# Optimization experiments

Measured on AMD Instinct MI355X. Metric: run time of the kernel, lower is better.

## Reference

```python
import jax, jax.numpy as jnp
import numpy as np

N, E, DIN, DOUT = 100000, 1600000, 64, 64
P_DROP = 0.1


def setup_inputs() -> dict:
    key = jax.random.key(0)
    k1, k2, k3 = jax.random.split(key, 3)
    x = jax.random.normal(k1, (N, DIN), dtype=jnp.float32)
    W = jax.random.normal(k2, (DIN, DOUT), dtype=jnp.float32) / np.sqrt(DIN)
    b = jnp.zeros((DOUT,), dtype=jnp.float32)
    edge_index = jax.random.randint(k3, (2, E), 0, N, dtype=jnp.int32)
    return {"x": x, "W": W, "b": b, "edge_index": edge_index}


def reference(x, W, b, edge_index):
    # PyG GCNConv semantics: add self-loops, symmetric normalization,
    # linear transform first, aggregate at target (edge_index[1]), bias after.
    row, col = edge_index[0], edge_index[1]
    loops = jnp.arange(N, dtype=edge_index.dtype)
    row = jnp.concatenate([row, loops])  # [E+N] source nodes
    col = jnp.concatenate([col, loops])  # [E+N] target nodes

    deg = jax.ops.segment_sum(jnp.ones_like(col, dtype=x.dtype), col, num_segments=N)
    dinv = jax.lax.rsqrt(jnp.maximum(deg, 1.0))  # self-loops guarantee deg >= 1
    norm = dinv[row] * dinv[col]  # [E+N]

    xw = x @ W  # [N, DOUT] small GEMM before scatter
    msg = xw[row] * norm[:, None]  # [E+N, DOUT] gather + scale
    agg = jax.ops.segment_sum(msg, col, num_segments=N) + b  # scatter-add

    h = jnp.tanh(agg)
    keep = jax.random.bernoulli(jax.random.key(42), 1.0 - P_DROP, h.shape)
    return jnp.where(keep, h / (1.0 - P_DROP), 0.0)
```

## Files before the change

### kernel.cpp

```cpp
#include <hip/hip_runtime.h>
#include <hip/hip_bf16.h>


#define NN 100000
#define NE 1600000
#define NBUCK 1563
#define P1B 256
#define P1T 1024
#define CHUNK 6250
#define CAP 1152
#define SPILLCAP 16384
#define HCAP 1536

typedef __attribute__((ext_vector_type(8))) short bf8;
typedef __attribute__((ext_vector_type(4))) float f32x4;

__device__ __forceinline__ unsigned rotl32(unsigned x, int r) {
    return (x << r) | (x >> (32 - r));
}

__device__ __forceinline__ void threefry2x32(unsigned k0, unsigned k1,
                                             unsigned x0, unsigned x1,
                                             unsigned& o0, unsigned& o1) {
    const unsigned ks0 = k0, ks1 = k1, ks2 = k0 ^ k1 ^ 0x1BD11BDAu;
    x0 += ks0; x1 += ks1;
    x0 += x1; x1 = rotl32(x1, 13); x1 ^= x0;
    x0 += x1; x1 = rotl32(x1, 15); x1 ^= x0;
    x0 += x1; x1 = rotl32(x1, 26); x1 ^= x0;
    x0 += x1; x1 = rotl32(x1, 6);  x1 ^= x0;
    x0 += ks1; x1 += ks2 + 1u;
    x0 += x1; x1 = rotl32(x1, 17); x1 ^= x0;
    x0 += x1; x1 = rotl32(x1, 29); x1 ^= x0;
    x0 += x1; x1 = rotl32(x1, 16); x1 ^= x0;
    x0 += x1; x1 = rotl32(x1, 24); x1 ^= x0;
    x0 += ks2; x1 += ks0 + 2u;
    x0 += x1; x1 = rotl32(x1, 13); x1 ^= x0;
    x0 += x1; x1 = rotl32(x1, 15); x1 ^= x0;
    x0 += x1; x1 = rotl32(x1, 26); x1 ^= x0;
    x0 += x1; x1 = rotl32(x1, 6);  x1 ^= x0;
    x0 += ks0; x1 += ks1 + 3u;
    x0 += x1; x1 = rotl32(x1, 17); x1 ^= x0;
    x0 += x1; x1 = rotl32(x1, 29); x1 ^= x0;
    x0 += x1; x1 = rotl32(x1, 16); x1 ^= x0;
    x0 += x1; x1 = rotl32(x1, 24); x1 ^= x0;
    x0 += ks1; x1 += ks2 + 4u;
    x0 += x1; x1 = rotl32(x1, 13); x1 ^= x0;
    x0 += x1; x1 = rotl32(x1, 15); x1 ^= x0;
    x0 += x1; x1 = rotl32(x1, 26); x1 ^= x0;
    x0 += x1; x1 = rotl32(x1, 6);  x1 ^= x0;
    x0 += ks2; x1 += ks0 + 5u;
    o0 = x0; o1 = x1;
}

__device__ __forceinline__ void sagg_finish(float4 a0, float4 a1, int lane,
                                            int c, float dv, float bv,
                                            float* __restrict__ out) {
    float ax = a0.x + a1.x, ay = a0.y + a1.y;
    float az = a0.z + a1.z, aw = a0.w + a1.w;
    ax += __shfl_xor(ax, 16); ax += __shfl_xor(ax, 32);
    ay += __shfl_xor(ay, 16); ay += __shfl_xor(ay, 32);
    az += __shfl_xor(az, 16); az += __shfl_xor(az, 32);
    aw += __shfl_xor(aw, 16); aw += __shfl_xor(aw, 32);
    const float sx = __shfl(ax, lane >> 2);
    const float sy = __shfl(ay, lane >> 2);
    const float sz = __shfl(az, lane >> 2);
    const float sw = __shfl(aw, lane >> 2);
    const float ab = (lane & 1) ? sy : sx;
    const float cd = (lane & 1) ? sw : sz;
    const float a = (lane & 2) ? cd : ab;
    const int p = c * 64 + lane;
    unsigned o0, o1;
    threefry2x32(0u, 42u, 0u, (unsigned)p, o0, o1);
    const unsigned bits = o0 ^ o1;
    const float u = __uint_as_float((bits >> 9) | 0x3f800000u) - 1.0f;
    const float h = tanhf(dv * a + bv);
    out[p] = (u < 0.9f) ? h / 0.9f : 0.0f;
}

#define UNPK4(v, A)                                                    \
    A.x += __uint_as_float((v).x << 16);                               \
    A.y += __uint_as_float((v).x & 0xffff0000u);                       \
    A.z += __uint_as_float((v).y << 16);                               \
    A.w += __uint_as_float((v).y & 0xffff0000u);

__global__ __launch_bounds__(P1T) void k_p1(const int* __restrict__ ei,
                                            int* __restrict__ gcur,
                                            unsigned* __restrict__ packed,
                                            unsigned* __restrict__ spill_pk,
                                            unsigned* __restrict__ spill_bk,
                                            int* __restrict__ gspill) {
    __shared__ int hb[NBUCK];
    __shared__ int lc[NBUCK];
    const int tid = threadIdx.x;
    for (int i = tid; i < NBUCK; i += P1T) { hb[i] = 0; lc[i] = 0; }
    __syncthreads();
    const int base = blockIdx.x * CHUNK;
    for (int i = tid; i < CHUNK; i += P1T) {
        const unsigned t = (unsigned)ei[NE + base + i];
        if (t < NN) atomicAdd(&hb[t >> 6], 1);
    }
    __syncthreads();
    for (int i = tid; i < NBUCK; i += P1T) {
        const int h = hb[i];
        hb[i] = h ? atomicAdd(&gcur[i], h) : 0;
        lc[i] = 0;
    }
    __syncthreads();
    for (int i = tid; i < CHUNK; i += P1T) {
        const unsigned t = (unsigned)ei[NE + base + i];
        if (t >= NN) continue;
        const unsigned src = (unsigned)ei[base + i];
        const int bk = t >> 6;
        const unsigned pk = src | ((t & 63u) << 17);
        const int pos = hb[bk] + atomicAdd(&lc[bk], 1);
        if (pos < CAP) {
            packed[(size_t)bk * CAP + pos] = pk;
        } else {
            const int sp = atomicAdd(gspill, 1);
            if (sp < SPILLCAP) { spill_pk[sp] = pk; spill_bk[sp] = (unsigned)bk; }
        }
    }
}

__global__ __launch_bounds__(256) void k_xw(const float* __restrict__ x,
                                            const float* __restrict__ W,
                                            const unsigned* __restrict__ packed,
                                            const int* __restrict__ gcur,
                                            const unsigned* __restrict__ spill_pk,
                                            const unsigned* __restrict__ spill_bk,
                                            const int* __restrict__ gspill,
                                            int* __restrict__ deg_g,
                                            __hip_bfloat16* __restrict__ xsh) {
    __shared__ unsigned short xbf[64 * 64];
    __shared__ unsigned short wb[64 * 64];
    __shared__ int hist[64];
    __shared__ float sdinv[64];
    const int tid = threadIdx.x;
    const int b = blockIdx.x;
    const int row0 = b * 64;
    const int nrow = (NN - row0) < 64 ? (NN - row0) : 64;
    for (int i = tid; i < 64 * 32; i += 256) {
        const int r = i >> 5, cp = i & 31;
        unsigned v = 0u;
        if (r < nrow) {
            const float2 xv = *(const float2*)(x + (size_t)(row0 + r) * 64 + 2 * cp);
            const __hip_bfloat16 b0 = __float2bfloat16(xv.x);
            const __hip_bfloat16 b1 = __float2bfloat16(xv.y);
            v = ((unsigned)*(const unsigned short*)&b1 << 16) |
                *(const unsigned short*)&b0;
        }
        *(unsigned*)((char*)xbf + ((r * 128 + cp * 4) ^ ((r & 7) << 4))) = v;
    }
    for (int i = tid; i < 64 * 64; i += 256) {
        const int k = i >> 6, d = i & 63;
        const __hip_bfloat16 wv = __float2bfloat16(W[i]);
        *(unsigned short*)((char*)wb + ((d * 128 + k * 2) ^ ((d & 7) << 4))) =
            *(const unsigned short*)&wv;
    }
    if (tid < 64) hist[tid] = 0;
    __syncthreads();
    {
        int cnt = gcur[b];
        cnt = (cnt < 0) ? 0 : (cnt > CAP ? CAP : cnt);
        const unsigned* __restrict__ seg = packed + (size_t)b * CAP;
        for (int i = tid; i < cnt; i += 256) atomicAdd(&hist[seg[i] >> 17], 1);
        int ns = *gspill;
        ns = (ns < 0) ? 0 : (ns > SPILLCAP ? SPILLCAP : ns);
        for (int i = tid; i < ns; i += 256)
            if ((int)spill_bk[i] == b) atomicAdd(&hist[(spill_pk[i] >> 17) & 63u], 1);
    }
    __syncthreads();
    if (tid < 64) {
        sdinv[tid] = rsqrtf(1.0f + (float)hist[tid]);
        const int myrow = row0 + tid;
        if (myrow < NN) deg_g[myrow] = hist[tid];
    }
    const int wid = tid >> 6, lane = tid & 63;
    const int m = lane & 15, kg = lane >> 4;
    f32x4 acc0 = {0.f, 0.f, 0.f, 0.f}, acc1 = {0.f, 0.f, 0.f, 0.f};
    f32x4 acc2 = {0.f, 0.f, 0.f, 0.f}, acc3 = {0.f, 0.f, 0.f, 0.f};
    const int arow = wid * 16 + m;
#pragma unroll
    for (int kk = 0; kk < 2; ++kk) {
        const int kbase = (kg * 8 + kk * 32) * 2;
        const bf8 af = *(const bf8*)((const char*)xbf +
                                     ((arow * 128 + kbase) ^ ((arow & 7) << 4)));
        const int d0 = 0 * 16 + m, d1 = 1 * 16 + m, d2 = 2 * 16 + m, d3 = 3 * 16 + m;
        const bf8 bf0 = *(const bf8*)((const char*)wb +
                                      ((d0 * 128 + kbase) ^ ((d0 & 7) << 4)));
        const bf8 bf1 = *(const bf8*)((const char*)wb +
                                      ((d1 * 128 + kbase) ^ ((d1 & 7) << 4)));
        const bf8 bf2 = *(const bf8*)((const char*)wb +
                                      ((d2 * 128 + kbase) ^ ((d2 & 7) << 4)));
        const bf8 bf3 = *(const bf8*)((const char*)wb +
                                      ((d3 * 128 + kbase) ^ ((d3 & 7) << 4)));
        acc0 = __builtin_amdgcn_mfma_f32_16x16x32_bf16(af, bf0, acc0, 0, 0, 0);
        acc1 = __builtin_amdgcn_mfma_f32_16x16x32_bf16(af, bf1, acc1, 0, 0, 0);
        acc2 = __builtin_amdgcn_mfma_f32_16x16x32_bf16(af, bf2, acc2, 0, 0, 0);
        acc3 = __builtin_amdgcn_mfma_f32_16x16x32_bf16(af, bf3, acc3, 0, 0, 0);
    }
    __syncthreads();
#pragma unroll
    for (int j = 0; j < 4; ++j) {
        const int r = wid * 16 + kg * 4 + j;
        const float dv = sdinv[r];
        const float v0 = acc0[j] * dv, v1 = acc1[j] * dv;
        const float v2 = acc2[j] * dv, v3 = acc3[j] * dv;
        const __hip_bfloat16 h0 = __float2bfloat16(v0);
        const __hip_bfloat16 h1 = __float2bfloat16(v1);
        const __hip_bfloat16 h2 = __float2bfloat16(v2);
        const __hip_bfloat16 h3 = __float2bfloat16(v3);
        xbf[r * 64 + 0 * 16 + m]  = *(const unsigned short*)&h0;
        xbf[r * 64 + 1 * 16 + m]  = *(const unsigned short*)&h1;
        xbf[r * 64 + 2 * 16 + m]  = *(const unsigned short*)&h2;
        xbf[r * 64 + 3 * 16 + m]  = *(const unsigned short*)&h3;
    }
    __syncthreads();
    {
        const uint4* __restrict__ src = (const uint4*)xbf;
        uint4* __restrict__ dst = (uint4*)(xsh + (size_t)row0 * 64);
        const int n16 = nrow * 8;
        for (int i = tid; i < n16; i += 256) dst[i] = src[i];
    }
}

__global__ __launch_bounds__(256) void k_sagg(const unsigned* __restrict__ packed,
                                              const int* __restrict__ gcur,
                                              const unsigned* __restrict__ spill_pk,
                                              const unsigned* __restrict__ spill_bk,
                                              const int* __restrict__ gspill,
                                              const int* __restrict__ deg_g,
                                              const __hip_bfloat16* __restrict__ xsh,
                                              const float* __restrict__ bias,
                                              float* __restrict__ out) {
    __shared__ unsigned sorted[HCAP];
    __shared__ int hist[32];
    __shared__ int pref[32];
    __shared__ int cur[32];
    __shared__ float sdinv[32];
    const int tid = threadIdx.x;
    const int b = blockIdx.x >> 1;
    const unsigned half = blockIdx.x & 1;
    int seg = gcur[b];
    seg = (seg < 0) ? 0 : (seg > CAP ? CAP : seg);
    const unsigned* __restrict__ region = packed + (size_t)b * CAP;
    int ns = *gspill;
    ns = (ns < 0) ? 0 : (ns > SPILLCAP ? SPILLCAP : ns);
    if (tid < 32) {
        const int c = b * 64 + (int)half * 32 + tid;
        hist[tid] = (c < NN) ? deg_g[c] : 0;
    }
    __syncthreads();
    if (tid == 0) {
        int run = 0;
        for (int t = 0; t < 32; ++t) { pref[t] = run; run += hist[t]; }
    }
    __syncthreads();
    const int hcnt = pref[31] + hist[31];
    const bool oversize = (hcnt > HCAP);
    if (tid < 32) {
        cur[tid] = pref[tid];
        sdinv[tid] = rsqrtf(1.0f + (float)hist[tid]);
    }
    __syncthreads();
    if (!oversize) {
        for (int i = tid; i < seg; i += 256) {
            const unsigned pk = region[i];
            if (((pk >> 22) & 1u) == half) {
                const int pos = atomicAdd(&cur[(pk >> 17) & 31u], 1);
                if (pos < HCAP) sorted[pos] = pk & 0x1FFFFu;
            }
        }
        for (int i = tid; i < ns; i += 256) {
            if ((int)spill_bk[i] == b) {
                const unsigned pk = spill_pk[i];
                if (((pk >> 22) & 1u) == half) {
                    const int pos = atomicAdd(&cur[(pk >> 17) & 31u], 1);
                    if (pos < HCAP) sorted[pos] = pk & 0x1FFFFu;
                }
            }
        }
    }
    __syncthreads();

    const int wid = tid >> 6, lane = tid & 63;
    const int q = lane >> 4, sl = lane & 15;
    const uint2* __restrict__ xs4 = (const uint2*)xsh;
    const float bv = bias[lane];
#pragma unroll 1
    for (int t = 0; t < 8; t += 2) {
        const int nlA = wid * 8 + t, nlB = nlA + 1;
        const int cA = b * 64 + (int)half * 32 + nlA;
        const int cB = cA + 1;
        if (cA >= NN) break;
        const bool hasB = (cB < NN);
        const int offA = pref[nlA], offB = pref[nlB];
        int degA = hist[nlA];
        degA = (degA < 0) ? 0 : (degA > hcnt ? hcnt : degA);
        int degB = hasB ? hist[nlB] : 0;
        degB = (degB < 0) ? 0 : (degB > hcnt ? hcnt : degB);
        float4 a0A = {0.f,0.f,0.f,0.f}, a1A = {0.f,0.f,0.f,0.f};
        float4 a0B = {0.f,0.f,0.f,0.f}, a1B = {0.f,0.f,0.f,0.f};
        if (q == 0) {
            const uint2 vA = xs4[(size_t)cA * 16 + sl];
            UNPK4(vA, a0A)
            if (hasB) {
                const uint2 vB = xs4[(size_t)cB * 16 + sl];
                UNPK4(vB, a0B)
            }
        }
        if (!oversize) {
            const int dmax = (degA > degB) ? degA : degB;
            for (int j = 0; j < dmax; j += 8) {
                const int e0 = j + q, e1 = j + 4 + q;
                uint2 v0A = {0u,0u}, v1A = {0u,0u}, v0B = {0u,0u}, v1B = {0u,0u};
                if (e0 < degA) v0A = xs4[(size_t)sorted[offA + e0] * 16 + sl];
                if (e1 < degA) v1A = xs4[(size_t)sorted[offA + e1] * 16 + sl];
                if (e0 < degB) v0B = xs4[(size_t)sorted[offB + e0] * 16 + sl];
                if (e1 < degB) v1B = xs4[(size_t)sorted[offB + e1] * 16 + sl];
                UNPK4(v0A, a0A)
                UNPK4(v1A, a1A)
                UNPK4(v0B, a0B)
                UNPK4(v1B, a1B)
            }
        } else {
            if (q == 0) {
                const unsigned tlA = (unsigned)((int)half * 32 + nlA);
                const unsigned tlB = tlA + 1u;
                for (int i = 0; i < seg; ++i) {
                    const unsigned pk = region[i];
                    const unsigned tl = pk >> 17;
                    if (tl == tlA) {
                        const uint2 v = xs4[(size_t)(pk & 0x1FFFFu) * 16 + sl];
                        UNPK4(v, a0A)
                    }
                    if (hasB && tl == tlB) {
                        const uint2 v = xs4[(size_t)(pk & 0x1FFFFu) * 16 + sl];
                        UNPK4(v, a0B)
                    }
                }
                for (int i = 0; i < ns; ++i) {
                    if ((int)spill_bk[i] == b) {
                        const unsigned pk = spill_pk[i];
                        const unsigned tl = pk >> 17;
                        if (tl == tlA) {
                            const uint2 v = xs4[(size_t)(pk & 0x1FFFFu) * 16 + sl];
                            UNPK4(v, a0A)
                        }
                        if (hasB && tl == tlB) {
                            const uint2 v = xs4[(size_t)(pk & 0x1FFFFu) * 16 + sl];
                            UNPK4(v, a0B)
                        }
                    }
                }
            }
        }
        sagg_finish(a0A, a1A, lane, cA, sdinv[nlA], bv, out);
        if (hasB) sagg_finish(a0B, a1B, lane, cB, sdinv[nlB], bv, out);
    }
}

extern "C" void kernel_launch(void* const* d_in, const int* in_sizes, int n_in,
                              void* d_out, int out_size, void* d_ws, size_t ws_size,
                              hipStream_t stream) {
    const float* x  = (const float*)d_in[0];
    const float* W  = (const float*)d_in[1];
    const float* b  = (const float*)d_in[2];
    const int*   ei = (const int*)d_in[3];
    float* out = (float*)d_out;

    __hip_bfloat16* xsh = (__hip_bfloat16*)d_ws;
    unsigned* packed = (unsigned*)(xsh + (size_t)NN * 64);
    int* gcur = (int*)(packed + (size_t)NBUCK * CAP);
    int* gspill = gcur + NBUCK;
    unsigned* spill_pk = (unsigned*)(gspill + 1);
    unsigned* spill_bk = spill_pk + SPILLCAP;
    int* deg_g = (int*)(spill_bk + SPILLCAP);

    hipMemsetAsync(gcur, 0, (NBUCK + 1) * sizeof(int), stream);
    k_p1<<<P1B, P1T, 0, stream>>>(ei, gcur, packed, spill_pk, spill_bk, gspill);
    k_xw<<<NBUCK, 256, 0, stream>>>(x, W, packed, gcur, spill_pk, spill_bk, gspill, deg_g, xsh);
    k_sagg<<<NBUCK * 2, 256, 0, stream>>>(packed, gcur, spill_pk, spill_bk, gspill, deg_g, xsh, b, out);
}
```

Baseline: 89.53 us.

## Bucket edges by 32 target nodes so aggregation blocks skip half-filtering

The partition pass now buckets edges into 32-node buckets instead of 64-node buckets. Each aggregation block owns one bucket directly, so it no longer scans a shared 64-node segment and discards the half belonging to its sibling block. The partition kernel also keeps each thread's source and target values in registers across its two passes instead of reloading edge_index from global memory. The degree-histogram kernel reads two buckets per 64-row tile. The smaller per-bucket capacity raises the chance of spilling to the slow serial spill path.

```diff
diff --git a/kernel.cpp b/kernel.cpp
--- a/kernel.cpp
+++ b/kernel.cpp
@@ -4,11 +4,12 @@
 
 #define NN 100000
 #define NE 1600000
-#define NBUCK 1563
+#define NB2 3125
 #define P1B 256
 #define P1T 1024
 #define CHUNK 6250
-#define CAP 1152
+#define NSLOT 7
+#define CAP 576
 #define SPILLCAP 16384
 #define HCAP 1536
 
@@ -89,29 +90,38 @@
                                             unsigned* __restrict__ spill_pk,
                                             unsigned* __restrict__ spill_bk,
                                             int* __restrict__ gspill) {
-    __shared__ int hb[NBUCK];
-    __shared__ int lc[NBUCK];
+    __shared__ int hb[NB2];
+    __shared__ int lc[NB2];
     const int tid = threadIdx.x;
-    for (int i = tid; i < NBUCK; i += P1T) { hb[i] = 0; lc[i] = 0; }
+    for (int i = tid; i < NB2; i += P1T) { hb[i] = 0; lc[i] = 0; }
     __syncthreads();
     const int base = blockIdx.x * CHUNK;
-    for (int i = tid; i < CHUNK; i += P1T) {
-        const unsigned t = (unsigned)ei[NE + base + i];
-        if (t < NN) atomicAdd(&hb[t >> 6], 1);
-    }
-    __syncthreads();
-    for (int i = tid; i < NBUCK; i += P1T) {
+    unsigned tc[NSLOT], sc[NSLOT];
+#pragma unroll
+    for (int k = 0; k < NSLOT; ++k) {
+        const int i = tid + k * P1T;
+        tc[k] = 0xFFFFFFFFu;
+        sc[k] = 0u;
+        if (i < CHUNK) {
+            const unsigned t = (unsigned)ei[NE + base + i];
+            tc[k] = t;
+            sc[k] = (unsigned)ei[base + i];
+            if (t < NN) atomicAdd(&hb[t >> 5], 1);
+        }
+    }
+    __syncthreads();
+    for (int i = tid; i < NB2; i += P1T) {
         const int h = hb[i];
         hb[i] = h ? atomicAdd(&gcur[i], h) : 0;
         lc[i] = 0;
     }
     __syncthreads();
-    for (int i = tid; i < CHUNK; i += P1T) {
-        const unsigned t = (unsigned)ei[NE + base + i];
+#pragma unroll
+    for (int k = 0; k < NSLOT; ++k) {
+        const unsigned t = tc[k];
         if (t >= NN) continue;
-        const unsigned src = (unsigned)ei[base + i];
-        const int bk = t >> 6;
-        const unsigned pk = src | ((t & 63u) << 17);
+        const int bk = (int)(t >> 5);
+        const unsigned pk = sc[k] | ((t & 63u) << 17);
         const int pos = hb[bk] + atomicAdd(&lc[bk], 1);
         if (pos < CAP) {
             packed[(size_t)bk * CAP + pos] = pk;
@@ -160,14 +170,21 @@
     if (tid < 64) hist[tid] = 0;
     __syncthreads();
     {
-        int cnt = gcur[b];
-        cnt = (cnt < 0) ? 0 : (cnt > CAP ? CAP : cnt);
-        const unsigned* __restrict__ seg = packed + (size_t)b * CAP;
-        for (int i = tid; i < cnt; i += 256) atomicAdd(&hist[seg[i] >> 17], 1);
+#pragma unroll 1
+        for (int h2 = 0; h2 < 2; ++h2) {
+            const int bk = 2 * b + h2;
+            if (bk >= NB2) break;
+            int cnt = gcur[bk];
+            cnt = (cnt < 0) ? 0 : (cnt > CAP ? CAP : cnt);
+            const unsigned* __restrict__ seg = packed + (size_t)bk * CAP;
+            for (int i = tid; i < cnt; i += 256)
+                atomicAdd(&hist[(seg[i] >> 17) & 63u], 1);
+        }
         int ns = *gspill;
         ns = (ns < 0) ? 0 : (ns > SPILLCAP ? SPILLCAP : ns);
         for (int i = tid; i < ns; i += 256)
-            if ((int)spill_bk[i] == b) atomicAdd(&hist[(spill_pk[i] >> 17) & 63u], 1);
+            if ((int)(spill_bk[i] >> 1) == b)
+                atomicAdd(&hist[(spill_pk[i] >> 17) & 63u], 1);
     }
     __syncthreads();
     if (tid < 64) {
@@ -204,16 +221,14 @@
     for (int j = 0; j < 4; ++j) {
         const int r = wid * 16 + kg * 4 + j;
         const float dv = sdinv[r];
-        const float v0 = acc0[j] * dv, v1 = acc1[j] * dv;
-        const float v2 = acc2[j] * dv, v3 = acc3[j] * dv;
-        const __hip_bfloat16 h0 = __float2bfloat16(v0);
-        const __hip_bfloat16 h1 = __float2bfloat16(v1);
-        const __hip_bfloat16 h2 = __float2bfloat16(v2);
-        const __hip_bfloat16 h3 = __float2bfloat16(v3);
-        xbf[r * 64 + 0 * 16 + m]  = *(const unsigned short*)&h0;
-        xbf[r * 64 + 1 * 16 + m]  = *(const unsigned short*)&h1;
-        xbf[r * 64 + 2 * 16 + m]  = *(const unsigned short*)&h2;
-        xbf[r * 64 + 3 * 16 + m]  = *(const unsigned short*)&h3;
+        const __hip_bfloat16 h0 = __float2bfloat16(acc0[j] * dv);
+        const __hip_bfloat16 h1 = __float2bfloat16(acc1[j] * dv);
+        const __hip_bfloat16 h2 = __float2bfloat16(acc2[j] * dv);
+        const __hip_bfloat16 h3 = __float2bfloat16(acc3[j] * dv);
+        xbf[r * 64 + 0 * 16 + m] = *(const unsigned short*)&h0;
+        xbf[r * 64 + 1 * 16 + m] = *(const unsigned short*)&h1;
+        xbf[r * 64 + 2 * 16 + m] = *(const unsigned short*)&h2;
+        xbf[r * 64 + 3 * 16 + m] = *(const unsigned short*)&h3;
     }
     __syncthreads();
     {
@@ -239,15 +254,14 @@
     __shared__ int cur[32];
     __shared__ float sdinv[32];
     const int tid = threadIdx.x;
-    const int b = blockIdx.x >> 1;
-    const unsigned half = blockIdx.x & 1;
+    const int b = blockIdx.x;
     int seg = gcur[b];
     seg = (seg < 0) ? 0 : (seg > CAP ? CAP : seg);
     const unsigned* __restrict__ region = packed + (size_t)b * CAP;
     int ns = *gspill;
     ns = (ns < 0) ? 0 : (ns > SPILLCAP ? SPILLCAP : ns);
     if (tid < 32) {
-        const int c = b * 64 + (int)half * 32 + tid;
+        const int c = b * 32 + tid;
         hist[tid] = (c < NN) ? deg_g[c] : 0;
     }
     __syncthreads();
@@ -266,18 +280,14 @@
     if (!oversize) {
         for (int i = tid; i < seg; i += 256) {
             const unsigned pk = region[i];
-            if (((pk >> 22) & 1u) == half) {
-                const int pos = atomicAdd(&cur[(pk >> 17) & 31u], 1);
-                if (pos < HCAP) sorted[pos] = pk & 0x1FFFFu;
-            }
+            const int pos = atomicAdd(&cur[(pk >> 17) & 31u], 1);
+            if (pos < HCAP) sorted[pos] = pk & 0x1FFFFu;
         }
         for (int i = tid; i < ns; i += 256) {
             if ((int)spill_bk[i] == b) {
                 const unsigned pk = spill_pk[i];
-                if (((pk >> 22) & 1u) == half) {
-                    const int pos = atomicAdd(&cur[(pk >> 17) & 31u], 1);
-                    if (pos < HCAP) sorted[pos] = pk & 0x1FFFFu;
-                }
+                const int pos = atomicAdd(&cur[(pk >> 17) & 31u], 1);
+                if (pos < HCAP) sorted[pos] = pk & 0x1FFFFu;
             }
         }
     }
@@ -290,7 +300,7 @@
 #pragma unroll 1
     for (int t = 0; t < 8; t += 2) {
         const int nlA = wid * 8 + t, nlB = nlA + 1;
-        const int cA = b * 64 + (int)half * 32 + nlA;
+        const int cA = b * 32 + nlA;
         const int cB = cA + 1;
         if (cA >= NN) break;
         const bool hasB = (cB < NN);
@@ -325,11 +335,11 @@
             }
         } else {
             if (q == 0) {
-                const unsigned tlA = (unsigned)((int)half * 32 + nlA);
+                const unsigned tlA = (unsigned)nlA;
                 const unsigned tlB = tlA + 1u;
                 for (int i = 0; i < seg; ++i) {
                     const unsigned pk = region[i];
-                    const unsigned tl = pk >> 17;
+                    const unsigned tl = (pk >> 17) & 31u;
                     if (tl == tlA) {
                         const uint2 v = xs4[(size_t)(pk & 0x1FFFFu) * 16 + sl];
                         UNPK4(v, a0A)
@@ -342,7 +352,7 @@
                 for (int i = 0; i < ns; ++i) {
                     if ((int)spill_bk[i] == b) {
                         const unsigned pk = spill_pk[i];
-                        const unsigned tl = pk >> 17;
+                        const unsigned tl = (pk >> 17) & 31u;
                         if (tl == tlA) {
                             const uint2 v = xs4[(size_t)(pk & 0x1FFFFu) * 16 + sl];
                             UNPK4(v, a0A)
@@ -371,14 +381,14 @@
 
     __hip_bfloat16* xsh = (__hip_bfloat16*)d_ws;
     unsigned* packed = (unsigned*)(xsh + (size_t)NN * 64);
-    int* gcur = (int*)(packed + (size_t)NBUCK * CAP);
-    int* gspill = gcur + NBUCK;
+    int* gcur = (int*)(packed + (size_t)NB2 * CAP);
+    int* gspill = gcur + NB2;
     unsigned* spill_pk = (unsigned*)(gspill + 1);
     unsigned* spill_bk = spill_pk + SPILLCAP;
     int* deg_g = (int*)(spill_bk + SPILLCAP);
 
-    hipMemsetAsync(gcur, 0, (NBUCK + 1) * sizeof(int), stream);
+    hipMemsetAsync(gcur, 0, (NB2 + 1) * sizeof(int), stream);
     k_p1<<<P1B, P1T, 0, stream>>>(ei, gcur, packed, spill_pk, spill_bk, gspill);
-    k_xw<<<NBUCK, 256, 0, stream>>>(x, W, packed, gcur, spill_pk, spill_bk, gspill, deg_g, xsh);
-    k_sagg<<<NBUCK * 2, 256, 0, stream>>>(packed, gcur, spill_pk, spill_bk, gspill, deg_g, xsh, b, out);
-}
+    k_xw<<<(NN + 63) / 64, 256, 0, stream>>>(x, W, packed, gcur, spill_pk, spill_bk, gspill, deg_g, xsh);
+    k_sagg<<<NB2, 256, 0, stream>>>(packed, gcur, spill_pk, spill_bk, gspill, deg_g, xsh, b, out);
+}
```

Measured after the change: 96.66 us. 8.0% more time.
